# Optimization experiments

Measured on AMD Instinct MI355X. Metric: run time of the kernel, lower is better.

## Reference

```python
import jax, jax.numpy as jnp
import numpy as np

D = 2048; H = 8; HD = 256; KV = 4; GHD = 512; GKV = 4; ROT = 128
F = 8192; V = 32000; B = 2; S = 1024; WIN = 512; EPS = 1e-6
THETA_S = 10000.0; THETA_G = 1000000.0


def _rms(x, w):
    return x * jax.lax.rsqrt(jnp.mean(x * x, axis=-1, keepdims=True) + EPS) * w


def _rms_ns(x):
    return x * jax.lax.rsqrt(jnp.mean(x * x, axis=-1, keepdims=True) + EPS)


def _angles(d, theta):
    # cos/sin tables: [S, d//2]
    inv = 1.0 / (theta ** (jnp.arange(0, d, 2, dtype=jnp.float32) / d))
    ang = jnp.arange(S, dtype=jnp.float32)[:, None] * inv[None, :]
    return jnp.cos(ang), jnp.sin(ang)


def _rope(x, cos, sin):
    # x: [B,S,H,d]; interleaved complex rotation on pairs
    b, s, h, d = x.shape
    xr = x.reshape(b, s, h, d // 2, 2)
    x1, x2 = xr[..., 0], xr[..., 1]
    c = cos[None, :, None, :]
    sn = sin[None, :, None, :]
    return jnp.stack([x1 * c - x2 * sn, x1 * sn + x2 * c], axis=-1).reshape(b, s, h, d)


def _partial_rope(x, cos, sin, rot):
    if rot == x.shape[-1]:
        return _rope(x, cos, sin)
    return jnp.concatenate([_rope(x[..., :rot], cos, sin), x[..., rot:]], axis=-1)


def _block(x, wq, wk, wv, wo, qn, kn, wg, wu, wd, ln1, ln2, ln3, ln4, scal,
           cos, sin, rot, mask, n_rep):
    res = x
    h = _rms(x, ln1)
    xq = jnp.einsum('bsd,dhc->bshc', h, wq)
    xk = jnp.einsum('bsd,dkc->bskc', h, wk)
    if wv is None:
        xv = _rms_ns(xk)  # global block: V = unscaled-RMS-normed K (pre k_norm)
    else:
        xv = _rms_ns(jnp.einsum('bsd,dkc->bskc', h, wv))
    xq = _rms(xq, qn)
    xk = _rms(xk, kn)
    xq = _partial_rope(xq, cos, sin, rot)
    xk = _partial_rope(xk, cos, sin, rot)
    q = xq.transpose(0, 2, 1, 3)  # [B,H,S,d]
    k = xk.transpose(0, 2, 1, 3)
    v = xv.transpose(0, 2, 1, 3)
    if n_rep != 1:
        k = jnp.repeat(k, n_rep, axis=1)
        v = jnp.repeat(v, n_rep, axis=1)
    scores = jnp.einsum('bhqd,bhkd->bhqk', q, k)  # NOTE: no 1/sqrt(d), as in source
    p = jax.nn.softmax(scores.astype(jnp.float32), axis=-1, where=mask[:, None, :, :]).astype(x.dtype)
    o = jnp.einsum('bhqk,bhkd->bhqd', p, v).transpose(0, 2, 1, 3)
    o = o.reshape(x.shape[0], x.shape[1], -1)
    o = _rms(jnp.einsum('bsd,do->bso', o, wo), ln2)
    x = res + o
    res = x
    hf = _rms(x, ln3)
    ffn = jnp.einsum('bsf,fd->bsd',
                     jax.nn.gelu(jnp.einsum('bsd,df->bsf', hf, wg), approximate=True)
                     * jnp.einsum('bsd,df->bsf', hf, wu), wd)
    x = res + _rms(ffn, ln4)
    return x * scal


def setup_inputs() -> dict:
    key = jax.random.key(0)
    ks = jax.random.split(key, 20)
    n = lambda k, shp: jax.random.normal(k, shp, jnp.float32) * 0.02
    inp = {
        'tokens': jax.random.randint(ks[0], (B, S), 0, V, jnp.int32),
        'true_lengths': jnp.full((B,), S, jnp.int32),
        'embed': n(ks[1], (V, D)),
        'norm_w': jnp.ones((D,), jnp.float32),
        's_wq': n(ks[2], (D, H, HD)), 's_wk': n(ks[3], (D, KV, HD)), 's_wv': n(ks[4], (D, KV, HD)),
        's_wo': n(ks[5], (H * HD, D)),
        's_qn': jnp.ones((HD,), jnp.float32), 's_kn': jnp.ones((HD,), jnp.float32),
        's_wg': n(ks[6], (D, F)), 's_wu': n(ks[7], (D, F)), 's_wd': n(ks[8], (F, D)),
        's_ln1': jnp.ones((D,), jnp.float32), 's_ln2': jnp.ones((D,), jnp.float32),
        's_ln3': jnp.ones((D,), jnp.float32), 's_ln4': jnp.ones((D,), jnp.float32),
        's_scal': jnp.ones((1,), jnp.float32),
        'g_wq': n(ks[9], (D, H, GHD)), 'g_wk': n(ks[10], (D, GKV, GHD)),
        'g_wo': n(ks[11], (H * GHD, D)),
        'g_qn': jnp.ones((GHD,), jnp.float32), 'g_kn': jnp.ones((GHD,), jnp.float32),
        'g_wg': n(ks[12], (D, F)), 'g_wu': n(ks[13], (D, F)), 'g_wd': n(ks[14], (F, D)),
        'g_ln1': jnp.ones((D,), jnp.float32), 'g_ln2': jnp.ones((D,), jnp.float32),
        'g_ln3': jnp.ones((D,), jnp.float32), 'g_ln4': jnp.ones((D,), jnp.float32),
        'g_scal': jnp.ones((1,), jnp.float32),
    }
    return inp


def reference(tokens, true_lengths, embed, norm_w,
              s_wq, s_wk, s_wv, s_wo, s_qn, s_kn, s_wg, s_wu, s_wd,
              s_ln1, s_ln2, s_ln3, s_ln4, s_scal,
              g_wq, g_wk, g_wo, g_qn, g_kn, g_wg, g_wu, g_wd,
              g_ln1, g_ln2, g_ln3, g_ln4, g_scal):
    # prefill from empty cache: seq_positions = 0, cache len == seqlen
    qpos = jnp.arange(S)[:, None]
    kpos = jnp.arange(S)[None, :]
    causal = qpos >= kpos
    sw = causal & ((qpos - kpos) < WIN)
    kvalid = kpos[None, 0, :][None, :] if False else (jnp.arange(S)[None, :] < true_lengths[:, None])  # [B,S]
    sliding_mask = sw[None, :, :] & kvalid[:, None, :]
    global_mask = causal[None, :, :] & kvalid[:, None, :]

    cos_s, sin_s = _angles(HD, THETA_S)
    cos_g, sin_g = _angles(ROT, THETA_G)

    h = embed[tokens] * jnp.sqrt(jnp.float32(D))
    h = _block(h, s_wq, s_wk, s_wv, s_wo, s_qn, s_kn, s_wg, s_wu, s_wd,
               s_ln1, s_ln2, s_ln3, s_ln4, s_scal, cos_s, sin_s, HD, sliding_mask, H // KV)
    h = _block(h, g_wq, g_wk, None, g_wo, g_qn, g_kn, g_wg, g_wu, g_wd,
               g_ln1, g_ln2, g_ln3, g_ln4, g_scal, cos_g, sin_g, ROT, global_mask, H // GKV)
    h = _rms(h, norm_w)
    logits = jnp.einsum('bsd,vd->bsv', h, embed)  # tied embedding head
    return logits
```

## Files before the change

### kernel.cpp

```cpp
#include <hip/hip_runtime.h>
#include <math.h>

typedef unsigned short u16;
typedef _Float16 f16;
typedef __attribute__((ext_vector_type(8))) short bf16x8;
typedef __attribute__((ext_vector_type(8))) _Float16 f16x8;
typedef __attribute__((ext_vector_type(4))) float f32x4;

constexpr int cB   = 2;
constexpr int cS   = 1024;
constexpr int cD   = 2048;
constexpr int cH   = 8;
constexpr int cHD  = 256;
constexpr int cKV  = 4;
constexpr int cGHD = 512;
constexpr int cGKV = 4;
constexpr int cROT = 128;
constexpr int cF   = 8192;
constexpr int cV   = 32000;
constexpr int cWIN = 512;
constexpr int cM   = cB * cS;
constexpr float cEPS = 1e-6f;
constexpr size_t MB = 1024 * 1024;

__device__ inline u16 f2bf(float x) {
    unsigned u = __float_as_uint(x);
    u += 0x7fff + ((u >> 16) & 1);
    return (u16)(u >> 16);
}
__device__ inline float bf2f(u16 v) { return __uint_as_float(((unsigned)v) << 16); }
__device__ inline void splitbf(float v, u16& h, u16& l) {
    h = f2bf(v);
    l = f2bf(v - bf2f(h));
}
__device__ inline u16 f2h(float x) { union { f16 h; u16 u; } c; c.h = (f16)x; return c.u; }
__device__ inline float h2f(u16 v) { union { u16 u; f16 h; } c; c.u = v; return (float)c.h; }

__device__ inline int swz16(int row, int chunk) {
    return row * 32 + ((chunk ^ ((row >> 1) & 3)) << 3);
}
__device__ inline int swzK(int row, int ch) {
    return row * 64 + ((ch ^ (row & 7)) << 3);
}

typedef __attribute__((address_space(1))) const unsigned int gu32;
typedef __attribute__((address_space(3))) unsigned int lu32;
__device__ inline void ldsload16(const u16* g, u16* l) {
    __builtin_amdgcn_global_load_lds((gu32*)g, (lu32*)l, 16, 0, 0);
}

__device__ inline float gelu_tanh(float v) {
    const float t = tanhf(0.7978845608028654f * (v + 0.044715f * v * v * v));
    return 0.5f * v * (1.f + t);
}

__global__ void embed_kernel(const int* __restrict__ tok,
                             const float* __restrict__ emb,
                             float* __restrict__ out) {
    const int row = blockIdx.x;
    const int t = tok[row];
    const float* e = emb + (size_t)t * cD;
    float* o = out + (size_t)row * cD;
    const float sc = sqrtf((float)cD);
    for (int d = threadIdx.x; d < cD; d += blockDim.x) o[d] = e[d] * sc;
}

__global__ void rms_kernel(const float* __restrict__ x,
                           const float* __restrict__ w,
                           float* __restrict__ out, int dim) {
    const int row = blockIdx.x;
    const float* xr = x + (size_t)row * dim;
    float* orow = out + (size_t)row * dim;
    float ss = 0.f;
    for (int d = threadIdx.x; d < dim; d += blockDim.x) { float v = xr[d]; ss += v * v; }
    for (int o = 32; o >= 1; o >>= 1) ss += __shfl_xor(ss, o);
    __shared__ float rb[8];
    if ((threadIdx.x & 63) == 0) rb[threadIdx.x >> 6] = ss;
    __syncthreads();
    ss = rb[0] + rb[1] + rb[2] + rb[3];
    const float r = rsqrtf(ss / dim + cEPS);
    for (int d = threadIdx.x; d < dim; d += blockDim.x)
        orow[d] = xr[d] * r * (w ? w[d] : 1.f);
}

__global__ void rms_f16_kernel(const float* __restrict__ x,
                               const float* __restrict__ w,
                               u16* __restrict__ out, int dim) {
    const int row = blockIdx.x;
    const float* xr = x + (size_t)row * dim;
    u16* orow = out + (size_t)row * dim;
    float ss = 0.f;
    for (int d = threadIdx.x; d < dim; d += blockDim.x) { float v = xr[d]; ss += v * v; }
    for (int o = 32; o >= 1; o >>= 1) ss += __shfl_xor(ss, o);
    __shared__ float rb[8];
    if ((threadIdx.x & 63) == 0) rb[threadIdx.x >> 6] = ss;
    __syncthreads();
    ss = rb[0] + rb[1] + rb[2] + rb[3];
    const float r = rsqrtf(ss / dim + cEPS);
    for (int d = threadIdx.x; d < dim; d += blockDim.x)
        orow[d] = f2h(xr[d] * r * (w ? w[d] : 1.f));
}

__global__ void rms_add_kernel(const float* __restrict__ res,
                               const float* __restrict__ x,
                               const float* __restrict__ w,
                               const float* __restrict__ scal,
                               float* __restrict__ out, int dim) {
    const int row = blockIdx.x;
    const float* xr = x + (size_t)row * dim;
    const float* rr = res + (size_t)row * dim;
    float* orow = out + (size_t)row * dim;
    float ss = 0.f;
    for (int d = threadIdx.x; d < dim; d += blockDim.x) { float v = xr[d]; ss += v * v; }
    for (int o = 32; o >= 1; o >>= 1) ss += __shfl_xor(ss, o);
    __shared__ float rb[8];
    if ((threadIdx.x & 63) == 0) rb[threadIdx.x >> 6] = ss;
    __syncthreads();
    ss = rb[0] + rb[1] + rb[2] + rb[3];
    const float r = rsqrtf(ss / dim + cEPS);
    const float sc = scal ? *scal : 1.f;
    for (int d = threadIdx.x; d < dim; d += blockDim.x)
        orow[d] = (rr[d] + xr[d] * r * w[d]) * sc;
}

__global__ void rope_kernel(float* __restrict__ x, int NH, int HDIM, int rot, float theta) {
    const int row = blockIdx.x;
    const int s = (row / NH) % cS;
    float* xr = x + (size_t)row * HDIM;
    const int half = rot >> 1;
    for (int i = threadIdx.x; i < half; i += blockDim.x) {
        const float inv = powf(theta, -(2.f * i) / (float)rot);
        const float ang = (float)s * inv;
        const float c = cosf(ang), sn = sinf(ang);
        const float x1 = xr[2 * i], x2 = xr[2 * i + 1];
        xr[2 * i]     = x1 * c - x2 * sn;
        xr[2 * i + 1] = x1 * sn + x2 * c;
    }
}

__global__ __launch_bounds__(256) void tcast_kernel(const float* __restrict__ in,
                                                    u16* __restrict__ out,
                                                    int K, int N, int ldin) {
    __shared__ float t[32][33];
    const int kt = blockIdx.y * 32, nt = blockIdx.x * 32;
    const int tx = threadIdx.x & 31, ty = threadIdx.x >> 5;
#pragma unroll
    for (int j = 0; j < 4; ++j)
        t[ty + j * 8][tx] = in[(size_t)(kt + ty + j * 8) * ldin + nt + tx];
    __syncthreads();
#pragma unroll
    for (int j = 0; j < 4; ++j)
        out[(size_t)(nt + ty + j * 8) * K + kt + tx] = f2h(t[tx][ty + j * 8]);
}

__global__ void cast_kernel(const float* __restrict__ in, u16* __restrict__ out,
                            int n, int ps) {
    const int i = blockIdx.x * blockDim.x + threadIdx.x;
    if (i * 4 >= n) return;
    const float4 v = *(const float4*)&in[(size_t)i * 4];
    u16 h[4], l[4];
    splitbf(v.x, h[0], l[0]); splitbf(v.y, h[1], l[1]);
    splitbf(v.z, h[2], l[2]); splitbf(v.w, h[3], l[3]);
    uint2 oh, ol;
    oh.x = (unsigned)h[0] | ((unsigned)h[1] << 16);
    oh.y = (unsigned)h[2] | ((unsigned)h[3] << 16);
    ol.x = (unsigned)l[0] | ((unsigned)l[1] << 16);
    ol.y = (unsigned)l[2] | ((unsigned)l[3] << 16);
    *(uint2*)&out[(size_t)i * 4] = oh;
    *(uint2*)&out[(size_t)ps + (size_t)i * 4] = ol;
}

__global__ __launch_bounds__(256) void vtrans_kernel(const float* __restrict__ V,
                                                     u16* __restrict__ Vt,
                                                     int HDIM, int KVH) {
    __shared__ float t[32][33];
    const int bk = blockIdx.z;
    const int b = bk / KVH, kh = bk % KVH;
    const int st = blockIdx.y * 32, dt = blockIdx.x * 32;
    const int tx = threadIdx.x & 31, ty = threadIdx.x >> 5;
#pragma unroll
    for (int j = 0; j < 4; ++j)
        t[ty + j * 8][tx] = V[((size_t)(b * cS + st + ty + j * 8) * KVH + kh) * HDIM + dt + tx];
    __syncthreads();
#pragma unroll
    for (int j = 0; j < 4; ++j)
        Vt[((size_t)bk * HDIM + dt + ty + j * 8) * cS + st + tx] = f2h(t[tx][ty + j * 8]);
}

template<bool F16_OUT, bool GELU>
__global__ __launch_bounds__(256) void gemm_f16(const u16* __restrict__ A,
                                                const u16* __restrict__ Bt,
                                                void* __restrict__ Cout,
                                                const u16* __restrict__ gate,
                                                int Mt, int K, int ldc) {
    __shared__ u16 As[128 * 32];
    __shared__ u16 Bs[128 * 32];
    const int nwg = gridDim.x;
    const int q8 = nwg >> 3;
    const int dd = blockIdx.x;
    const int wk = (dd & 7) * q8 + (dd >> 3);
    const int bm = (wk % Mt) * 128;
    const int bn = (wk / Mt) * 128;
    const int tid = threadIdx.x;
    const int lane = tid & 63;
    const int wv = tid >> 6;
    const int wr = (wv >> 1) * 64, wc = (wv & 1) * 64;
    const int r15 = lane & 15, hi16 = lane >> 4;

    f32x4 acc[4][4];
#pragma unroll
    for (int m = 0; m < 4; ++m)
#pragma unroll
        for (int n = 0; n < 4; ++n) acc[m][n] = (f32x4){0.f, 0.f, 0.f, 0.f};

    int rowS[2], koS[2];
#pragma unroll
    for (int i = 0; i < 2; ++i) {
        const int s = i * 256 + tid;
        rowS[i] = s >> 2;
        koS[i] = ((s & 3) ^ ((rowS[i] >> 1) & 3)) * 8;
    }
    u16* ldsA0 = &As[(wv * 64) * 8];
    u16* ldsA1 = &As[(256 + wv * 64) * 8];
    u16* ldsB0 = &Bs[(wv * 64) * 8];
    u16* ldsB1 = &Bs[(256 + wv * 64) * 8];

    for (int k0 = 0; k0 < K; k0 += 32) {
        __syncthreads();
        ldsload16(&A [(size_t)(bm + rowS[0]) * K + k0 + koS[0]], ldsA0);
        ldsload16(&A [(size_t)(bm + rowS[1]) * K + k0 + koS[1]], ldsA1);
        ldsload16(&Bt[(size_t)(bn + rowS[0]) * K + k0 + koS[0]], ldsB0);
        ldsload16(&Bt[(size_t)(bn + rowS[1]) * K + k0 + koS[1]], ldsB1);
        __syncthreads();
        f16x8 af[4], bf4[4];
#pragma unroll
        for (int m = 0; m < 4; ++m)
            af[m] = *(const f16x8*)&As[swz16(wr + m * 16 + r15, hi16)];
#pragma unroll
        for (int n = 0; n < 4; ++n)
            bf4[n] = *(const f16x8*)&Bs[swz16(wc + n * 16 + r15, hi16)];
#pragma unroll
        for (int m = 0; m < 4; ++m)
#pragma unroll
            for (int n = 0; n < 4; ++n)
                acc[m][n] = __builtin_amdgcn_mfma_f32_16x16x32_f16(af[m], bf4[n], acc[m][n], 0, 0, 0);
    }
#pragma unroll
    for (int m = 0; m < 4; ++m)
#pragma unroll
        for (int n = 0; n < 4; ++n)
#pragma unroll
            for (int r = 0; r < 4; ++r) {
                const int row = bm + wr + m * 16 + hi16 * 4 + r;
                const int col = bn + wc + n * 16 + r15;
                const size_t idx = (size_t)row * ldc + col;
                float v = acc[m][n][r];
                if (GELU) v = gelu_tanh(h2f(gate[idx])) * v;
                if (F16_OUT) ((u16*)Cout)[idx] = f2h(v);
                else         ((float*)Cout)[idx] = v;
            }
}

__global__ __launch_bounds__(256) void gemm_logits(const u16* __restrict__ A,
                                                   const float* __restrict__ Bf,
                                                   float* __restrict__ Cout,
                                                   int Mt, int K, int ldc) {
    __shared__ u16 As[128 * 32];
    __shared__ u16 Bs[128 * 32];
    const int nwg = gridDim.x;
    const int q8 = nwg >> 3;
    const int dd = blockIdx.x;
    const int wk = (dd & 7) * q8 + (dd >> 3);
    const int bm = (wk % Mt) * 128;
    const int bn = (wk / Mt) * 128;
    const int tid = threadIdx.x;
    const int lane = tid & 63;
    const int wv = tid >> 6;
    const int wr = (wv >> 1) * 64, wc = (wv & 1) * 64;
    const int r15 = lane & 15, hi16 = lane >> 4;

    f32x4 acc[4][4];
#pragma unroll
    for (int m = 0; m < 4; ++m)
#pragma unroll
        for (int n = 0; n < 4; ++n) acc[m][n] = (f32x4){0.f, 0.f, 0.f, 0.f};

    int rowS[2], koS[2];
#pragma unroll
    for (int i = 0; i < 2; ++i) {
        const int s = i * 256 + tid;
        rowS[i] = s >> 2;
        koS[i] = ((s & 3) ^ ((rowS[i] >> 1) & 3)) * 8;
    }
    u16* ldsA0 = &As[(wv * 64) * 8];
    u16* ldsA1 = &As[(256 + wv * 64) * 8];

    int rowB[4], fB[4], wB[4];
#pragma unroll
    for (int j = 0; j < 4; ++j) {
        const int c = tid + j * 256;
        rowB[j] = c >> 3; fB[j] = c & 7;
        wB[j] = swz16(rowB[j], fB[j] >> 1) + (fB[j] & 1) * 4;
    }
    float4 fv[4];
#pragma unroll
    for (int j = 0; j < 4; ++j)
        fv[j] = *(const float4*)&Bf[(size_t)(bn + rowB[j]) * K + fB[j] * 4];

    for (int k0 = 0; k0 < K; k0 += 32) {
        __syncthreads();
        ldsload16(&A[(size_t)(bm + rowS[0]) * K + k0 + koS[0]], ldsA0);
        ldsload16(&A[(size_t)(bm + rowS[1]) * K + k0 + koS[1]], ldsA1);
#pragma unroll
        for (int j = 0; j < 4; ++j) {
            uint2 p;
            p.x = (unsigned)f2h(fv[j].x) | ((unsigned)f2h(fv[j].y) << 16);
            p.y = (unsigned)f2h(fv[j].z) | ((unsigned)f2h(fv[j].w) << 16);
            *(uint2*)&Bs[wB[j]] = p;
        }
        __syncthreads();
        if (k0 + 32 < K) {
#pragma unroll
            for (int j = 0; j < 4; ++j)
                fv[j] = *(const float4*)&Bf[(size_t)(bn + rowB[j]) * K + k0 + 32 + fB[j] * 4];
        }
        f16x8 af[4], bf4[4];
#pragma unroll
        for (int m = 0; m < 4; ++m)
            af[m] = *(const f16x8*)&As[swz16(wr + m * 16 + r15, hi16)];
#pragma unroll
        for (int n = 0; n < 4; ++n)
            bf4[n] = *(const f16x8*)&Bs[swz16(wc + n * 16 + r15, hi16)];
#pragma unroll
        for (int m = 0; m < 4; ++m)
#pragma unroll
            for (int n = 0; n < 4; ++n)
                acc[m][n] = __builtin_amdgcn_mfma_f32_16x16x32_f16(af[m], bf4[n], acc[m][n], 0, 0, 0);
    }
#pragma unroll
    for (int m = 0; m < 4; ++m)
#pragma unroll
        for (int n = 0; n < 4; ++n)
#pragma unroll
            for (int r = 0; r < 4; ++r)
                Cout[(size_t)(bm + wr + m * 16 + hi16 * 4 + r) * ldc
                     + bn + wc + n * 16 + r15] = acc[m][n][r];
}

__global__ __launch_bounds__(256) void qk_kernel(const u16* __restrict__ Qb, int qps,
                                                 const u16* __restrict__ Kb, int kps,
                                                 float* __restrict__ Sc,
                                                 int HDIM, int KVH, int win) {
    const int bm = blockIdx.y * 128;
    const int bn = blockIdx.x * 128;
    if (bn > bm + 127) return;
    if (win > 0 && bm - bn > win + 126) return;
    const int bh = blockIdx.z;
    const int b = bh / cH, h = bh % cH;
    const int kh = h / (cH / KVH);

    __shared__ u16 As[2][128 * 32];
    __shared__ u16 Bs[2][128 * 32];
    const int tid = threadIdx.x;
    const int lane = tid & 63;
    const int w = tid >> 6;
    const int wr = (w >> 1) * 64, wc = (w & 1) * 64;
    const int r15 = lane & 15, hi16 = lane >> 4;

    const int lda = cH * HDIM, ldb = KVH * HDIM;
    const u16* Aq = Qb + ((size_t)b * cS * cH + h) * HDIM;
    const u16* Bk = Kb + ((size_t)b * cS * KVH + kh) * HDIM;

    f32x4 acc[4][4];
#pragma unroll
    for (int m = 0; m < 4; ++m)
#pragma unroll
        for (int n = 0; n < 4; ++n) acc[m][n] = (f32x4){0.f, 0.f, 0.f, 0.f};

    const int c0 = tid, c1 = tid + 256;
    const int ar0 = c0 >> 2, ak0 = (c0 & 3) * 8;
    const int ar1 = c1 >> 2, ak1 = (c1 & 3) * 8;
    const int w0 = swz16(ar0, c0 & 3), w1 = swz16(ar1, c1 & 3);

    for (int k0 = 0; k0 < HDIM; k0 += 32) {
        uint4 v0 = *(const uint4*)&Aq[(size_t)(bm + ar0) * lda + k0 + ak0];
        uint4 v1 = *(const uint4*)&Aq[(size_t)(bm + ar1) * lda + k0 + ak1];
        uint4 v2 = *(const uint4*)&Aq[(size_t)qps + (size_t)(bm + ar0) * lda + k0 + ak0];
        uint4 v3 = *(const uint4*)&Aq[(size_t)qps + (size_t)(bm + ar1) * lda + k0 + ak1];
        uint4 v4 = *(const uint4*)&Bk[(size_t)(bn + ar0) * ldb + k0 + ak0];
        uint4 v5 = *(const uint4*)&Bk[(size_t)(bn + ar1) * ldb + k0 + ak1];
        uint4 v6 = *(const uint4*)&Bk[(size_t)kps + (size_t)(bn + ar0) * ldb + k0 + ak0];
        uint4 v7 = *(const uint4*)&Bk[(size_t)kps + (size_t)(bn + ar1) * ldb + k0 + ak1];
        __syncthreads();
        *(uint4*)&As[0][w0] = v0;
        *(uint4*)&As[0][w1] = v1;
        *(uint4*)&As[1][w0] = v2;
        *(uint4*)&As[1][w1] = v3;
        *(uint4*)&Bs[0][w0] = v4;
        *(uint4*)&Bs[0][w1] = v5;
        *(uint4*)&Bs[1][w0] = v6;
        *(uint4*)&Bs[1][w1] = v7;
        __syncthreads();
        bf16x8 ah[4], al[4], bh4[4], bl4[4];
#pragma unroll
        for (int m = 0; m < 4; ++m) {
            const int o = swz16(wr + m * 16 + r15, hi16);
            ah[m] = *(const bf16x8*)&As[0][o];
            al[m] = *(const bf16x8*)&As[1][o];
        }
#pragma unroll
        for (int n = 0; n < 4; ++n) {
            const int o = swz16(wc + n * 16 + r15, hi16);
            bh4[n] = *(const bf16x8*)&Bs[0][o];
            bl4[n] = *(const bf16x8*)&Bs[1][o];
        }
#pragma unroll
        for (int m = 0; m < 4; ++m)
#pragma unroll
            for (int n = 0; n < 4; ++n) {
                acc[m][n] = __builtin_amdgcn_mfma_f32_16x16x32_bf16(ah[m], bl4[n], acc[m][n], 0, 0, 0);
                acc[m][n] = __builtin_amdgcn_mfma_f32_16x16x32_bf16(al[m], bh4[n], acc[m][n], 0, 0, 0);
                acc[m][n] = __builtin_amdgcn_mfma_f32_16x16x32_bf16(ah[m], bh4[n], acc[m][n], 0, 0, 0);
            }
    }
    float* Crow = Sc + (size_t)bh * cS * cS;
#pragma unroll
    for (int m = 0; m < 4; ++m)
#pragma unroll
        for (int n = 0; n < 4; ++n)
#pragma unroll
            for (int r = 0; r < 4; ++r)
                Crow[(size_t)(bm + wr + m * 16 + hi16 * 4 + r) * cS + bn + wc + n * 16 + r15]
                    = acc[m][n][r];
}

__global__ __launch_bounds__(256) void softmax_kernel(float* __restrict__ Sc,
                                                      const int* __restrict__ tlen,
                                                      int win) {
    const int q = blockIdx.x, bh = blockIdx.y, b = bh / cH;
    float* row = Sc + ((size_t)bh * cS + q) * cS;
    u16* rowh = (u16*)row;
    const int tid = threadIdx.x;
    const int tl = tlen[b];
    const int kmax = min(q, tl - 1);
    const int kmin = (win > 0) ? max(0, q - win + 1) : 0;

    float v[4];
    float m = -1e30f;
#pragma unroll
    for (int j = 0; j < 4; ++j) {
        const int k = tid + j * 256;
        const bool ok = (k >= kmin && k <= kmax);
        v[j] = ok ? row[k] : -1e30f;
        m = fmaxf(m, v[j]);
    }
    for (int o = 32; o >= 1; o >>= 1) m = fmaxf(m, __shfl_xor(m, o));
    __shared__ float rb[8];
    if ((tid & 63) == 0) rb[tid >> 6] = m;
    __syncthreads();
    m = fmaxf(fmaxf(rb[0], rb[1]), fmaxf(rb[2], rb[3]));

    float e[4];
    float s = 0.f;
#pragma unroll
    for (int j = 0; j < 4; ++j) {
        const int k = tid + j * 256;
        const bool ok = (k >= kmin && k <= kmax);
        e[j] = ok ? expf(v[j] - m) : 0.f;
        s += e[j];
    }
    for (int o = 32; o >= 1; o >>= 1) s += __shfl_xor(s, o);
    __shared__ float sb[4];
    if ((tid & 63) == 0) sb[tid >> 6] = s;
    __syncthreads();
    s = sb[0] + sb[1] + sb[2] + sb[3];
    const float inv = 1.f / s;
    __syncthreads();
#pragma unroll
    for (int j = 0; j < 4; ++j) {
        const int k = tid + j * 256;
        rowh[k] = f2h(e[j] * inv);
    }
}

__global__ __launch_bounds__(256) void pv_f16(const u16* __restrict__ P,
                                              const u16* __restrict__ Vt,
                                              u16* __restrict__ O,
                                              int HDIM, int KVH, int win) {
    const int bh = blockIdx.z;
    const int b = bh / cH, h = bh % cH;
    const int kh = h / (cH / KVH);
    const int bm = blockIdx.y * 128;
    const int bn = blockIdx.x * 128;

    __shared__ u16 As[128 * 64];
    __shared__ u16 Bs[128 * 64];
    const int tid = threadIdx.x;
    const int lane = tid & 63;
    const int w = tid >> 6;
    const int wr = (w >> 1) * 64, wc = (w & 1) * 64;
    const int r15 = lane & 15, hi16 = lane >> 4;

    const u16* Ap = P + (size_t)bh * cS * 2048;
    const u16* Bv = Vt + ((size_t)b * KVH + kh) * HDIM * cS;

    f32x4 acc[4][4];
#pragma unroll
    for (int m = 0; m < 4; ++m)
#pragma unroll
        for (int n = 0; n < 4; ++n) acc[m][n] = (f32x4){0.f, 0.f, 0.f, 0.f};

    int rA[4], cA[4], wl[4];
#pragma unroll
    for (int j = 0; j < 4; ++j) {
        const int c = tid + j * 256;
        rA[j] = c >> 3; cA[j] = (c & 7) * 8;
        wl[j] = swzK(rA[j], c & 7);
    }

    const int klo = (win > 0) ? (max(0, bm - win + 1) & ~63) : 0;
    const int khi = min(bm + 128, cS);

    for (int k0 = klo; k0 < khi; k0 += 64) {
        uint4 av[4], bv[4];
#pragma unroll
        for (int j = 0; j < 4; ++j) {
            av[j] = *(const uint4*)&Ap[(size_t)(bm + rA[j]) * 2048 + k0 + cA[j]];
            bv[j] = *(const uint4*)&Bv[(size_t)(bn + rA[j]) * cS + k0 + cA[j]];
        }
        __syncthreads();
#pragma unroll
        for (int j = 0; j < 4; ++j) {
            *(uint4*)&As[wl[j]] = av[j];
            *(uint4*)&Bs[wl[j]] = bv[j];
        }
        __syncthreads();
#pragma unroll
        for (int kk = 0; kk < 2; ++kk) {
            f16x8 af[4], bf4[4];
#pragma unroll
            for (int m = 0; m < 4; ++m)
                af[m] = *(const f16x8*)&As[swzK(wr + m * 16 + r15, kk * 4 + hi16)];
#pragma unroll
            for (int n = 0; n < 4; ++n)
                bf4[n] = *(const f16x8*)&Bs[swzK(wc + n * 16 + r15, kk * 4 + hi16)];
#pragma unroll
            for (int m = 0; m < 4; ++m)
#pragma unroll
                for (int n = 0; n < 4; ++n)
                    acc[m][n] = __builtin_amdgcn_mfma_f32_16x16x32_f16(af[m], bf4[n], acc[m][n], 0, 0, 0);
        }
    }
    const int ldo = cH * HDIM;
#pragma unroll
    for (int m = 0; m < 4; ++m)
#pragma unroll
        for (int n = 0; n < 4; ++n)
#pragma unroll
            for (int r = 0; r < 4; ++r) {
                const int q = bm + wr + m * 16 + hi16 * 4 + r;
                const int d = bn + wc + n * 16 + r15;
                O[(size_t)(b * cS + q) * ldo + h * HDIM + d] = f2h(acc[m][n][r]);
            }
}

extern "C" void kernel_launch(void* const* d_in, const int* in_sizes, int n_in,
                              void* d_out, int out_size, void* d_ws, size_t ws_size,
                              hipStream_t stream) {
    (void)in_sizes; (void)n_in; (void)out_size; (void)ws_size;
    const int*   tokens = (const int*)  d_in[0];
    const int*   tlen   = (const int*)  d_in[1];
    const float* embed  = (const float*)d_in[2];
    const float* norm_w = (const float*)d_in[3];
    const float* s_wq   = (const float*)d_in[4];
    const float* s_wk   = (const float*)d_in[5];
    const float* s_wv   = (const float*)d_in[6];
    const float* s_wo   = (const float*)d_in[7];
    const float* s_qn   = (const float*)d_in[8];
    const float* s_kn   = (const float*)d_in[9];
    const float* s_wg   = (const float*)d_in[10];
    const float* s_wu   = (const float*)d_in[11];
    const float* s_wd   = (const float*)d_in[12];
    const float* s_ln1  = (const float*)d_in[13];
    const float* s_ln2  = (const float*)d_in[14];
    const float* s_ln3  = (const float*)d_in[15];
    const float* s_ln4  = (const float*)d_in[16];
    const float* s_scal = (const float*)d_in[17];
    const float* g_wq   = (const float*)d_in[18];
    const float* g_wk   = (const float*)d_in[19];
    const float* g_wo   = (const float*)d_in[20];
    const float* g_qn   = (const float*)d_in[21];
    const float* g_kn   = (const float*)d_in[22];
    const float* g_wg   = (const float*)d_in[23];
    const float* g_wu   = (const float*)d_in[24];
    const float* g_wd   = (const float*)d_in[25];
    const float* g_ln1  = (const float*)d_in[26];
    const float* g_ln2  = (const float*)d_in[27];
    const float* g_ln3  = (const float*)d_in[28];
    const float* g_ln4  = (const float*)d_in[29];
    const float* g_scal = (const float*)d_in[30];

    char* w8 = (char*)d_ws;
    float* x   = (float*)(w8);
    u16*   ab  = (u16*)(w8 + 16 * MB);
    u16*   wp  = (u16*)(w8 + 24 * MB);
    u16*   Qb  = (u16*)(w8 + 24 * MB);
    u16*   Ob  = (u16*)(w8 + 24 * MB);
    u16*   t0b = (u16*)(w8 + 56 * MB);
    u16*   Kb  = (u16*)(w8 + 58 * MB);
    u16*   Vt  = (u16*)(w8 + 75 * MB);
    float* scores = (float*)(w8 + 84 * MB);
    u16*   Pb  = (u16*)(w8 + 84 * MB);
    float* qf  = (float*)(w8 + 84 * MB);
    u16*   wo2 = (u16*)(w8 + 84 * MB);
    u16*   t1b = (u16*)(w8 + 88 * MB);
    float* kf  = (float*)(w8 + 116 * MB);
    float* r0  = (float*)(w8 + 116 * MB);
    float* fo  = (float*)(w8 + 120 * MB);
    float* vf  = (float*)(w8 + 132 * MB);

    auto tcast = [&](const float* in, u16* outp, int K, int N, int ldin) {
        tcast_kernel<<<dim3(N / 32, K / 32), 256, 0, stream>>>(in, outp, K, N, ldin);
    };
    auto gemmF = [&](const u16* A, const u16* Bt, float* C, int N, int K, int ldc) {
        gemm_f16<false, false><<<16 * (N / 128), 256, 0, stream>>>(A, Bt, C, nullptr, 16, K, ldc);
    };
    auto gemmH = [&](const u16* A, const u16* Bt, u16* C, int N, int K, int ldc) {
        gemm_f16<true, false><<<16 * (N / 128), 256, 0, stream>>>(A, Bt, C, nullptr, 16, K, ldc);
    };
    auto gemmHG = [&](const u16* A, const u16* Bt, u16* C, const u16* gate,
                      int N, int K, int ldc) {
        gemm_f16<true, true><<<16 * (N / 128), 256, 0, stream>>>(A, Bt, C, gate, 16, K, ldc);
    };

    auto attention = [&](int HDIM, int KVH, int win) {
        const int qn = cM * cH * HDIM;
        const int kn = cM * KVH * HDIM;
        cast_kernel<<<(qn / 4 + 255) / 256, 256, 0, stream>>>(qf, Qb, qn, qn);
        cast_kernel<<<(kn / 4 + 255) / 256, 256, 0, stream>>>(kf, Kb, kn, kn);
        vtrans_kernel<<<dim3(HDIM / 32, cS / 32, cB * KVH), 256, 0, stream>>>(vf, Vt, HDIM, KVH);
        qk_kernel<<<dim3(cS / 128, cS / 128, cB * cH), 256, 0, stream>>>(
            Qb, qn, Kb, kn, scores, HDIM, KVH, win);
        softmax_kernel<<<dim3(cS, cB * cH), 256, 0, stream>>>(scores, tlen, win);
        pv_f16<<<dim3(HDIM / 128, cS / 128, cB * cH), 256, 0, stream>>>(
            Pb, Vt, Ob, HDIM, KVH, win);
    };

    embed_kernel<<<cM, 256, 0, stream>>>(tokens, embed, x);

    rms_f16_kernel<<<cM, 256, 0, stream>>>(x, s_ln1, ab, cD);
    tcast(s_wq, wp, cD, cH * cHD, cH * cHD);
    gemmF(ab, wp, qf, cH * cHD, cD, cH * cHD);
    tcast(s_wk, wp, cD, cKV * cHD, cKV * cHD);
    gemmF(ab, wp, kf, cKV * cHD, cD, cKV * cHD);
    tcast(s_wv, wp, cD, cKV * cHD, cKV * cHD);
    gemmF(ab, wp, vf, cKV * cHD, cD, cKV * cHD);
    rms_kernel<<<cM * cKV, 256, 0, stream>>>(vf, nullptr, vf, cHD);
    rms_kernel<<<cM * cH, 256, 0, stream>>>(qf, s_qn, qf, cHD);
    rms_kernel<<<cM * cKV, 256, 0, stream>>>(kf, s_kn, kf, cHD);
    rope_kernel<<<cM * cH, 128, 0, stream>>>(qf, cH, cHD, cHD, 10000.f);
    rope_kernel<<<cM * cKV, 128, 0, stream>>>(kf, cKV, cHD, cHD, 10000.f);
    attention(cHD, cKV, cWIN);
    tcast(s_wo, wo2, cH * cHD, cD, cD);
    gemmF(Ob, wo2, r0, cD, cH * cHD, cD);
    rms_add_kernel<<<cM, 256, 0, stream>>>(x, r0, s_ln2, nullptr, x, cD);
    rms_f16_kernel<<<cM, 256, 0, stream>>>(x, s_ln3, ab, cD);
    tcast(s_wg, wp, cD, cF, cF);
    gemmH(ab, wp, t1b, cF, cD, cF);
    tcast(s_wu, wp, cD, cF, cF);
    gemmHG(ab, wp, t0b, t1b, cF, cD, cF);
    tcast(s_wd, wp, cF, cD, cD);
    gemmF(t0b, wp, fo, cD, cF, cD);
    rms_add_kernel<<<cM, 256, 0, stream>>>(x, fo, s_ln4, s_scal, x, cD);

    rms_f16_kernel<<<cM, 256, 0, stream>>>(x, g_ln1, ab, cD);
    tcast(g_wq, wp, cD, cH * cGHD, cH * cGHD);
    gemmF(ab, wp, qf, cH * cGHD, cD, cH * cGHD);
    tcast(g_wk, wp, cD, cGKV * cGHD, cGKV * cGHD);
    gemmF(ab, wp, kf, cGKV * cGHD, cD, cGKV * cGHD);
    rms_kernel<<<cM * cGKV, 256, 0, stream>>>(kf, nullptr, vf, cGHD);
    rms_kernel<<<cM * cH, 256, 0, stream>>>(qf, g_qn, qf, cGHD);
    rms_kernel<<<cM * cGKV, 256, 0, stream>>>(kf, g_kn, kf, cGHD);
    rope_kernel<<<cM * cH, 64, 0, stream>>>(qf, cH, cGHD, cROT, 1000000.f);
    rope_kernel<<<cM * cGKV, 64, 0, stream>>>(kf, cGKV, cGHD, cROT, 1000000.f);
    attention(cGHD, cGKV, 0);
    tcast(g_wo, wo2, cH * cGHD, cD, cD);
    gemmF(Ob, wo2, r0, cD, cH * cGHD, cD);
    rms_add_kernel<<<cM, 256, 0, stream>>>(x, r0, g_ln2, nullptr, x, cD);
    rms_f16_kernel<<<cM, 256, 0, stream>>>(x, g_ln3, ab, cD);
    tcast(g_wg, wp, cD, cF, cF);
    gemmH(ab, wp, t1b, cF, cD, cF);
    tcast(g_wu, wp, cD, cF, cF);
    gemmHG(ab, wp, t0b, t1b, cF, cD, cF);
    tcast(g_wd, wp, cF, cD, cD);
    gemmF(t0b, wp, fo, cD, cF, cD);
    rms_add_kernel<<<cM, 256, 0, stream>>>(x, fo, g_ln4, g_scal, x, cD);

    rms_f16_kernel<<<cM, 256, 0, stream>>>(x, norm_w, ab, cD);
    gemm_logits<<<16 * (cV / 128), 256, 0, stream>>>(ab, embed, (float*)d_out, 16, cD, cV);
}
```

Before: 2.342 ms.

## Fuse residual-add with next RMSNorm, fuse QK norm with RoPE and casts, simplify logits

Merges the residual add-norm with the following RMSNorm into one addnorm kernel, and fuses the q/k RMSNorm, RoPE and hi/lo bf16 split cast into a single rmsrope kernel. This removes several launches and full round trips of activations through memory. The logits path now casts the embedding to f16 up front and reuses the generic gemm_f16 instead of a dedicated kernel that converted f32 weights inside the loop. The separate cast costs an extra pass over the 32000x2048 embedding.

After: 2.227 ms. -4.9%, faster.

```diff
diff --git a/kernel.cpp b/kernel.cpp
--- a/kernel.cpp
+++ b/kernel.cpp
@@ -101,40 +101,96 @@
         orow[d] = f2h(xr[d] * r * (w ? w[d] : 1.f));
 }
 
-__global__ void rms_add_kernel(const float* __restrict__ res,
-                               const float* __restrict__ x,
-                               const float* __restrict__ w,
-                               const float* __restrict__ scal,
-                               float* __restrict__ out, int dim) {
+__global__ __launch_bounds__(256) void addnorm_kernel(const float* __restrict__ res,
+                                                      const float* __restrict__ y,
+                                                      const float* __restrict__ w_add,
+                                                      const float* __restrict__ scal,
+                                                      const float* __restrict__ w_norm,
+                                                      float* __restrict__ xout,
+                                                      u16* __restrict__ abo) {
     const int row = blockIdx.x;
-    const float* xr = x + (size_t)row * dim;
-    const float* rr = res + (size_t)row * dim;
-    float* orow = out + (size_t)row * dim;
+    const float* yr = y + (size_t)row * cD;
+    const float* rr = res + (size_t)row * cD;
+    float* xo = xout + (size_t)row * cD;
+    u16* ao = abo + (size_t)row * cD;
+    const int tid = threadIdx.x;
+    __shared__ float rb[4];
+
+    float yl[8], xl[8];
     float ss = 0.f;
-    for (int d = threadIdx.x; d < dim; d += blockDim.x) { float v = xr[d]; ss += v * v; }
+#pragma unroll
+    for (int j = 0; j < 8; ++j) { yl[j] = yr[tid + j * 256]; ss += yl[j] * yl[j]; }
     for (int o = 32; o >= 1; o >>= 1) ss += __shfl_xor(ss, o);
-    __shared__ float rb[8];
-    if ((threadIdx.x & 63) == 0) rb[threadIdx.x >> 6] = ss;
+    if ((tid & 63) == 0) rb[tid >> 6] = ss;
     __syncthreads();
     ss = rb[0] + rb[1] + rb[2] + rb[3];
-    const float r = rsqrtf(ss / dim + cEPS);
+    const float r1 = rsqrtf(ss / cD + cEPS);
     const float sc = scal ? *scal : 1.f;
-    for (int d = threadIdx.x; d < dim; d += blockDim.x)
-        orow[d] = (rr[d] + xr[d] * r * w[d]) * sc;
-}
-
-__global__ void rope_kernel(float* __restrict__ x, int NH, int HDIM, int rot, float theta) {
+
+    float ss2 = 0.f;
+#pragma unroll
+    for (int j = 0; j < 8; ++j) {
+        const int d = tid + j * 256;
+        xl[j] = (rr[d] + yl[j] * r1 * w_add[d]) * sc;
+        ss2 += xl[j] * xl[j];
+    }
+    for (int o = 32; o >= 1; o >>= 1) ss2 += __shfl_xor(ss2, o);
+    __syncthreads();
+    if ((tid & 63) == 0) rb[tid >> 6] = ss2;
+    __syncthreads();
+    ss2 = rb[0] + rb[1] + rb[2] + rb[3];
+    const float r2 = rsqrtf(ss2 / cD + cEPS);
+#pragma unroll
+    for (int j = 0; j < 8; ++j) {
+        const int d = tid + j * 256;
+        xo[d] = xl[j];
+        ao[d] = f2h(xl[j] * r2 * w_norm[d]);
+    }
+}
+
+__global__ __launch_bounds__(128) void rmsrope_kernel(const float* __restrict__ x,
+                                                      const float* __restrict__ w,
+                                                      u16* __restrict__ out, int ps,
+                                                      int NH, int HDIM, int rot,
+                                                      float theta) {
     const int row = blockIdx.x;
     const int s = (row / NH) % cS;
-    float* xr = x + (size_t)row * HDIM;
-    const int half = rot >> 1;
-    for (int i = threadIdx.x; i < half; i += blockDim.x) {
-        const float inv = powf(theta, -(2.f * i) / (float)rot);
-        const float ang = (float)s * inv;
-        const float c = cosf(ang), sn = sinf(ang);
-        const float x1 = xr[2 * i], x2 = xr[2 * i + 1];
-        xr[2 * i]     = x1 * c - x2 * sn;
-        xr[2 * i + 1] = x1 * sn + x2 * c;
+    const float* xr = x + (size_t)row * HDIM;
+    u16* orow = out + (size_t)row * HDIM;
+    const int tid = threadIdx.x;
+    const int np = HDIM >> 1;
+    __shared__ float rb[2];
+
+    float v1[2], v2[2];
+    float ss = 0.f;
+    for (int p = tid, j = 0; p < np; p += 128, ++j) {
+        v1[j] = xr[2 * p]; v2[j] = xr[2 * p + 1];
+        ss += v1[j] * v1[j] + v2[j] * v2[j];
+    }
+    for (int o = 32; o >= 1; o >>= 1) ss += __shfl_xor(ss, o);
+    if ((tid & 63) == 0) rb[tid >> 6] = ss;
+    __syncthreads();
+    ss = rb[0] + rb[1];
+    const float r = rsqrtf(ss / HDIM + cEPS);
+    const int halfrot = rot >> 1;
+    for (int p = tid, j = 0; p < np; p += 128, ++j) {
+        const float a = v1[j] * r * w[2 * p];
+        const float b = v2[j] * r * w[2 * p + 1];
+        float o1 = a, o2 = b;
+        if (p < halfrot) {
+            const float inv = powf(theta, -(2.f * p) / (float)rot);
+            const float ang = (float)s * inv;
+            const float c = cosf(ang), sn = sinf(ang);
+            o1 = a * c - b * sn;
+            o2 = a * sn + b * c;
+        }
+        u16 hh, ll;
+        splitbf(o1, hh, ll);
+        orow[2 * p] = hh;
+        orow[(size_t)ps + 2 * p] = ll;
+        splitbf(o2, hh, ll);
+        orow[2 * p + 1] = hh;
+        orow[(size_t)ps + 2 * p + 1] = ll;
     }
 }
 
@@ -153,21 +209,15 @@
         out[(size_t)(nt + ty + j * 8) * K + kt + tx] = f2h(t[tx][ty + j * 8]);
 }
 
-__global__ void cast_kernel(const float* __restrict__ in, u16* __restrict__ out,
-                            int n, int ps) {
+__global__ void cast_f16_kernel(const float* __restrict__ in, u16* __restrict__ out,
+                                int n) {
     const int i = blockIdx.x * blockDim.x + threadIdx.x;
     if (i * 4 >= n) return;
     const float4 v = *(const float4*)&in[(size_t)i * 4];
-    u16 h[4], l[4];
-    splitbf(v.x, h[0], l[0]); splitbf(v.y, h[1], l[1]);
-    splitbf(v.z, h[2], l[2]); splitbf(v.w, h[3], l[3]);
-    uint2 oh, ol;
-    oh.x = (unsigned)h[0] | ((unsigned)h[1] << 16);
-    oh.y = (unsigned)h[2] | ((unsigned)h[3] << 16);
-    ol.x = (unsigned)l[0] | ((unsigned)l[1] << 16);
-    ol.y = (unsigned)l[2] | ((unsigned)l[3] << 16);
-    *(uint2*)&out[(size_t)i * 4] = oh;
-    *(uint2*)&out[(size_t)ps + (size_t)i * 4] = ol;
+    uint2 o;
+    o.x = (unsigned)f2h(v.x) | ((unsigned)f2h(v.y) << 16);
+    o.y = (unsigned)f2h(v.z) | ((unsigned)f2h(v.w) << 16);
+    *(uint2*)&out[(size_t)i * 4] = o;
 }
 
 __global__ __launch_bounds__(256) void vtrans_kernel(const float* __restrict__ V,
@@ -259,92 +309,6 @@
                 if (F16_OUT) ((u16*)Cout)[idx] = f2h(v);
                 else         ((float*)Cout)[idx] = v;
             }
-}
-
-__global__ __launch_bounds__(256) void gemm_logits(const u16* __restrict__ A,
-                                                   const float* __restrict__ Bf,
-                                                   float* __restrict__ Cout,
-                                                   int Mt, int K, int ldc) {
-    __shared__ u16 As[128 * 32];
-    __shared__ u16 Bs[128 * 32];
-    const int nwg = gridDim.x;
-    const int q8 = nwg >> 3;
-    const int dd = blockIdx.x;
-    const int wk = (dd & 7) * q8 + (dd >> 3);
-    const int bm = (wk % Mt) * 128;
-    const int bn = (wk / Mt) * 128;
-    const int tid = threadIdx.x;
-    const int lane = tid & 63;
-    const int wv = tid >> 6;
-    const int wr = (wv >> 1) * 64, wc = (wv & 1) * 64;
-    const int r15 = lane & 15, hi16 = lane >> 4;
-
-    f32x4 acc[4][4];
-#pragma unroll
-    for (int m = 0; m < 4; ++m)
-#pragma unroll
-        for (int n = 0; n < 4; ++n) acc[m][n] = (f32x4){0.f, 0.f, 0.f, 0.f};
-
-    int rowS[2], koS[2];
-#pragma unroll
-    for (int i = 0; i < 2; ++i) {
-        const int s = i * 256 + tid;
-        rowS[i] = s >> 2;
-        koS[i] = ((s & 3) ^ ((rowS[i] >> 1) & 3)) * 8;
-    }
-    u16* ldsA0 = &As[(wv * 64) * 8];
-    u16* ldsA1 = &As[(256 + wv * 64) * 8];
-
-    int rowB[4], fB[4], wB[4];
-#pragma unroll
-    for (int j = 0; j < 4; ++j) {
-        const int c = tid + j * 256;
-        rowB[j] = c >> 3; fB[j] = c & 7;
-        wB[j] = swz16(rowB[j], fB[j] >> 1) + (fB[j] & 1) * 4;
-    }
-    float4 fv[4];
-#pragma unroll
-    for (int j = 0; j < 4; ++j)
-        fv[j] = *(const float4*)&Bf[(size_t)(bn + rowB[j]) * K + fB[j] * 4];
-
-    for (int k0 = 0; k0 < K; k0 += 32) {
-        __syncthreads();
-        ldsload16(&A[(size_t)(bm + rowS[0]) * K + k0 + koS[0]], ldsA0);
-        ldsload16(&A[(size_t)(bm + rowS[1]) * K + k0 + koS[1]], ldsA1);
-#pragma unroll
-        for (int j = 0; j < 4; ++j) {
-            uint2 p;
-            p.x = (unsigned)f2h(fv[j].x) | ((unsigned)f2h(fv[j].y) << 16);
-            p.y = (unsigned)f2h(fv[j].z) | ((unsigned)f2h(fv[j].w) << 16);
-            *(uint2*)&Bs[wB[j]] = p;
-        }
-        __syncthreads();
-        if (k0 + 32 < K) {
-#pragma unroll
-            for (int j = 0; j < 4; ++j)
-                fv[j] = *(const float4*)&Bf[(size_t)(bn + rowB[j]) * K + k0 + 32 + fB[j] * 4];
-        }
-        f16x8 af[4], bf4[4];
-#pragma unroll
-        for (int m = 0; m < 4; ++m)
-            af[m] = *(const f16x8*)&As[swz16(wr + m * 16 + r15, hi16)];
-#pragma unroll
-        for (int n = 0; n < 4; ++n)
-            bf4[n] = *(const f16x8*)&Bs[swz16(wc + n * 16 + r15, hi16)];
-#pragma unroll
-        for (int m = 0; m < 4; ++m)
-#pragma unroll
-            for (int n = 0; n < 4; ++n)
-                acc[m][n] = __builtin_amdgcn_mfma_f32_16x16x32_f16(af[m], bf4[n], acc[m][n], 0, 0, 0);
-    }
-#pragma unroll
-    for (int m = 0; m < 4; ++m)
-#pragma unroll
-        for (int n = 0; n < 4; ++n)
-#pragma unroll
-            for (int r = 0; r < 4; ++r)
-                Cout[(size_t)(bm + wr + m * 16 + hi16 * 4 + r) * ldc
-                     + bn + wc + n * 16 + r15] = acc[m][n][r];
 }
 
 __global__ __launch_bounds__(256) void qk_kernel(const u16* __restrict__ Qb, int qps,
@@ -606,6 +570,7 @@
     u16*   wp  = (u16*)(w8 + 24 * MB);
     u16*   Qb  = (u16*)(w8 + 24 * MB);
     u16*   Ob  = (u16*)(w8 + 24 * MB);
+    u16*   embH= (u16*)(w8 + 24 * MB);
     u16*   t0b = (u16*)(w8 + 56 * MB);
     u16*   Kb  = (u16*)(w8 + 58 * MB);
     u16*   Vt  = (u16*)(w8 + 75 * MB);
@@ -636,8 +601,6 @@
     auto attention = [&](int HDIM, int KVH, int win) {
         const int qn = cM * cH * HDIM;
         const int kn = cM * KVH * HDIM;
-        cast_kernel<<<(qn / 4 + 255) / 256, 256, 0, stream>>>(qf, Qb, qn, qn);
-        cast_kernel<<<(kn / 4 + 255) / 256, 256, 0, stream>>>(kf, Kb, kn, kn);
         vtrans_kernel<<<dim3(HDIM / 32, cS / 32, cB * KVH), 256, 0, stream>>>(vf, Vt, HDIM, KVH);
         qk_kernel<<<dim3(cS / 128, cS / 128, cB * cH), 256, 0, stream>>>(
             Qb, qn, Kb, kn, scores, HDIM, KVH, win);
@@ -656,46 +619,44 @@
     tcast(s_wv, wp, cD, cKV * cHD, cKV * cHD);
     gemmF(ab, wp, vf, cKV * cHD, cD, cKV * cHD);
     rms_kernel<<<cM * cKV, 256, 0, stream>>>(vf, nullptr, vf, cHD);
-    rms_kernel<<<cM * cH, 256, 0, stream>>>(qf, s_qn, qf, cHD);
-    rms_kernel<<<cM * cKV, 256, 0, stream>>>(kf, s_kn, kf, cHD);
-    rope_kernel<<<cM * cH, 128, 0, stream>>>(qf, cH, cHD, cHD, 10000.f);
-    rope_kernel<<<cM * cKV, 128, 0, stream>>>(kf, cKV, cHD, cHD, 10000.f);
+    rmsrope_kernel<<<cM * cH, 128, 0, stream>>>(qf, s_qn, Qb, cM * cH * cHD,
+                                                cH, cHD, cHD, 10000.f);
+    rmsrope_kernel<<<cM * cKV, 128, 0, stream>>>(kf, s_kn, Kb, cM * cKV * cHD,
+                                                 cKV, cHD, cHD, 10000.f);
     attention(cHD, cKV, cWIN);
     tcast(s_wo, wo2, cH * cHD, cD, cD);
     gemmF(Ob, wo2, r0, cD, cH * cHD, cD);
-    rms_add_kernel<<<cM, 256, 0, stream>>>(x, r0, s_ln2, nullptr, x, cD);
-    rms_f16_kernel<<<cM, 256, 0, stream>>>(x, s_ln3, ab, cD);
+    addnorm_kernel<<<cM, 256, 0, stream>>>(x, r0, s_ln2, nullptr, s_ln3, x, ab);
     tcast(s_wg, wp, cD, cF, cF);
     gemmH(ab, wp, t1b, cF, cD, cF);
     tcast(s_wu, wp, cD, cF, cF);
     gemmHG(ab, wp, t0b, t1b, cF, cD, cF);
     tcast(s_wd, wp, cF, cD, cD);
     gemmF(t0b, wp, fo, cD, cF, cD);
-    rms_add_kernel<<<cM, 256, 0, stream>>>(x, fo, s_ln4, s_scal, x, cD);
-
-    rms_f16_kernel<<<cM, 256, 0, stream>>>(x, g_ln1, ab, cD);
+    addnorm_kernel<<<cM, 256, 0, stream>>>(x, fo, s_ln4, s_scal, g_ln1, x, ab);
+
     tcast(g_wq, wp, cD, cH * cGHD, cH * cGHD);
     gemmF(ab, wp, qf, cH * cGHD, cD, cH * cGHD);
     tcast(g_wk, wp, cD, cGKV * cGHD, cGKV * cGHD);
     gemmF(ab, wp, kf, cGKV * cGHD, cD, cGKV * cGHD);
     rms_kernel<<<cM * cGKV, 256, 0, stream>>>(kf, nullptr, vf, cGHD);
-    rms_kernel<<<cM * cH, 256, 0, stream>>>(qf, g_qn, qf, cGHD);
-    rms_kernel<<<cM * cGKV, 256, 0, stream>>>(kf, g_kn, kf, cGHD);
-    rope_kernel<<<cM * cH, 64, 0, stream>>>(qf, cH, cGHD, cROT, 1000000.f);
-    rope_kernel<<<cM * cGKV, 64, 0, stream>>>(kf, cGKV, cGHD, cROT, 1000000.f);
+    rmsrope_kernel<<<cM * cH, 128, 0, stream>>>(qf, g_qn, Qb, cM * cH * cGHD,
+                                                cH, cGHD, cROT, 1000000.f);
+    rmsrope_kernel<<<cM * cGKV, 128, 0, stream>>>(kf, g_kn, Kb, cM * cGKV * cGHD,
+                                                  cGKV, cGHD, cROT, 1000000.f);
     attention(cGHD, cGKV, 0);
     tcast(g_wo, wo2, cH * cGHD, cD, cD);
     gemmF(Ob, wo2, r0, cD, cH * cGHD, cD);
-    rms_add_kernel<<<cM, 256, 0, stream>>>(x, r0, g_ln2, nullptr, x, cD);
-    rms_f16_kernel<<<cM, 256, 0, stream>>>(x, g_ln3, ab, cD);
+    addnorm_kernel<<<cM, 256, 0, stream>>>(x, r0, g_ln2, nullptr, g_ln3, x, ab);
     tcast(g_wg, wp, cD, cF, cF);
     gemmH(ab, wp, t1b, cF, cD, cF);
     tcast(g_wu, wp, cD, cF, cF);
     gemmHG(ab, wp, t0b, t1b, cF, cD, cF);
     tcast(g_wd, wp, cF, cD, cD);
     gemmF(t0b, wp, fo, cD, cF, cD);
-    rms_add_kernel<<<cM, 256, 0, stream>>>(x, fo, g_ln4, g_scal, x, cD);
-
-    rms_f16_kernel<<<cM, 256, 0, stream>>>(x, norm_w, ab, cD);
-    gemm_logits<<<16 * (cV / 128), 256, 0, stream>>>(ab, embed, (float*)d_out, 16, cD, cV);
-}
+    addnorm_kernel<<<cM, 256, 0, stream>>>(x, fo, g_ln4, g_scal, norm_w, x, ab);
+
+    cast_f16_kernel<<<(cV * cD / 4 + 255) / 256, 256, 0, stream>>>(embed, embH, cV * cD);
+    gemm_f16<false, false><<<16 * (cV / 128), 256, 0, stream>>>(
+        ab, embH, (float*)d_out, nullptr, 16, cD, cV);
+}
```
